# Kernel tuning notes

Measured on AMD Instinct MI355X. Metric: run time of the kernel, lower is better.

The kernel has to match this reference:

```python
import jax, jax.numpy as jnp
import numpy as np

B, L, H, NH = 2, 512, 128, 2
DH = H // NH
POS_VOCAB, REL_VOCAB = 512, 257


def setup_inputs() -> dict:
    key = jax.random.key(0)
    ks = jax.random.split(key, 16)
    s = 0.02
    inp = {
        "query": jax.random.normal(ks[0], (B, L, H), jnp.float32),
        "key": jax.random.normal(ks[1], (B, L, H), jnp.float32),
        "value": jax.random.normal(ks[2], (B, L, H), jnp.float32),
        "Wq": jax.random.normal(ks[3], (H, H), jnp.float32) * s,
        "bq": jnp.zeros((H,), jnp.float32),
        "Wk": jax.random.normal(ks[4], (H, H), jnp.float32) * s,
        "bk": jnp.zeros((H,), jnp.float32),
        "Wv": jax.random.normal(ks[5], (H, H), jnp.float32) * s,
        "bv": jnp.zeros((H,), jnp.float32),
        "Wo": jax.random.normal(ks[6], (H, H), jnp.float32) * s,
        "bo": jnp.zeros((H,), jnp.float32),
        "E_PK": jax.random.normal(ks[7], (POS_VOCAB, H), jnp.float32) * s,
        "E_PV": jax.random.normal(ks[8], (POS_VOCAB, H), jnp.float32) * s,
        "E_RK": jax.random.normal(ks[9], (REL_VOCAB, H), jnp.float32) * s,
        "E_RV": jax.random.normal(ks[10], (REL_VOCAB, H), jnp.float32) * s,
        "poss_seq": jax.random.randint(ks[11], (B, L), 0, POS_VOCAB),
        "interval_seq": jax.random.randint(ks[12], (B, L, L), 0, REL_VOCAB),
        # causal mask (True = attend), same role as attn_mask in the torch module
        "attn_mask": jnp.broadcast_to(jnp.tril(jnp.ones((L, L), bool)), (B, L, L)),
    }
    return inp


def reference(query, key, value, Wq, bq, Wk, bk, Wv, bv, Wo, bo,
              E_PK, E_PV, E_RK, E_RV, poss_seq, interval_seq, attn_mask):
    b, l, _ = query.shape
    # linear projections (torch Linear: x @ W.T + b)
    Q = query @ Wq.T + bq
    K = key @ Wk.T + bk + E_PK[poss_seq]
    V = value @ Wv.T + bv + E_PV[poss_seq]
    # relative key/value embeddings: (b, l, l, h, dh) -> (b, h, l, l, dh)
    rel_k = E_RK[interval_seq].reshape(b, l, l, NH, DH).transpose(0, 3, 1, 2, 4)
    rel_v = E_RV[interval_seq].reshape(b, l, l, NH, DH).transpose(0, 3, 1, 2, 4)
    # split heads: (b, h, l, dh)
    Qh = Q.reshape(b, l, NH, DH).transpose(0, 2, 1, 3)
    Kh = K.reshape(b, l, NH, DH).transpose(0, 2, 1, 3)
    Vh = V.reshape(b, l, NH, DH).transpose(0, 2, 1, 3)
    scores = jnp.einsum('bhld,bhkd->bhlk', Qh, Kh)
    scores = scores + jnp.einsum('bhld,bhlkd->bhlk', Qh, rel_k)
    scores = scores / jnp.sqrt(jnp.float32(DH))
    m = attn_mask[:, None]  # (b, 1, l, l)
    scores = jnp.where(m, scores, -jnp.inf)
    w = jax.nn.softmax(scores, axis=-1)
    w = jnp.where(m, w, 0.0)
    out = jnp.einsum('bhlk,bhkd->bhld', w, Vh)
    out = out + jnp.einsum('bhlk,bhlkd->bhld', w, rel_v)
    out = out.transpose(0, 2, 1, 3).reshape(b, l, H)
    out = out @ Wo.T + bo
    out = jnp.where(jnp.isnan(out), 0.0, out)
    return out
```

## Files before the change

### kernel.cpp

```cpp
#include <hip/hip_runtime.h>
#include <math.h>

#define LL 512
#define HH 128
#define NHH 2
#define DHH 64
#define RELV 257
#define PKS  260

#define OFF_QH   0
#define OFF_KT   131072
#define OFF_VH   262144
#define OFF_PK   393216
#define OFF_WQT  925696
#define OFF_WKT  942080
#define OFF_WVT  958464
#define OFF_WOT  974848
#define OFF_ERKT 991232

__global__ void prep_kernel(const float* Wq, const float* Wk, const float* Wv,
                            const float* Wo, const float* E_RK, float* ws) {
    int g = blockIdx.x * 256 + threadIdx.x;
    if (g < 65536) {
        int m = g >> 14, rem = g & 16383, i = rem >> 7, j = rem & 127;
        const float* W = (m == 0) ? Wq : (m == 1) ? Wk : (m == 2) ? Wv : Wo;
        ws[OFF_WQT + m * 16384 + i * 128 + j] = W[j * 128 + i];
    } else if (g < 65536 + 128 * RELV) {
        int g2 = g - 65536;
        int hd = g2 / RELV, r = g2 - hd * RELV;
        ws[OFF_ERKT + hd * RELV + r] = E_RK[r * HH + hd];
    }
}

__launch_bounds__(512)
__global__ void qkv_kernel(const float* q_in, const float* k_in, const float* v_in,
                           const float* bq, const float* bk, const float* bv,
                           const float* E_PK, const float* E_PV, const int* poss,
                           const float* Wqt, const float* Wkt, const float* Wvt,
                           const float* ERKt,
                           float* Qh, float* Kt, float* Vh, float* PK) {
    int row0 = blockIdx.x * 4;
    int b = row0 >> 9;
    int l0 = row0 & 511;
    int t = threadIdx.x;

    __shared__ float xin[3][4][128];
    __shared__ float qr[4][128];

    for (int g = t; g < 1536; g += 512) {
        int m = g >> 9, rem = g & 511, rr = rem >> 7, i = rem & 127;
        const float* src = (m == 0) ? q_in : (m == 1) ? k_in : v_in;
        xin[m][rr][i] = src[(row0 + rr) * 128 + i];
    }
    __syncthreads();

    int j = t & 127, rr = t >> 7;
    int row = row0 + rr, l = l0 + rr;
    float aq = bq[j], ak = bk[j], av = bv[j];
    const float* xq = xin[0][rr];
    const float* xk = xin[1][rr];
    const float* xv = xin[2][rr];
#pragma unroll 8
    for (int i = 0; i < 128; i++) {
        aq += xq[i] * Wqt[i * 128 + j];
        ak += xk[i] * Wkt[i * 128 + j];
        av += xv[i] * Wvt[i * 128 + j];
    }
    int pos = poss[row];
    ak += E_PK[pos * 128 + j];
    av += E_PV[pos * 128 + j];

    int h = j >> 6, d = j & 63, bh = b * NHH + h;
    Qh[(bh * LL + l) * DHH + d] = aq;
    Vh[(bh * LL + l) * DHH + d] = av;
    Kt[(bh * DHH + d) * LL + l] = ak;
    qr[rr][j] = aq;
    __syncthreads();

    for (int idx = t; idx < 2 * RELV; idx += 512) {
        int hh = idx >= RELV;
        int r = idx - hh * RELV;
        const float* er = ERKt + hh * 64 * RELV + r;
        const float* q0 = qr[0] + hh * 64;
        const float* q1 = qr[1] + hh * 64;
        const float* q2v = qr[2] + hh * 64;
        const float* q3 = qr[3] + hh * 64;
        float a0 = 0.f, a1 = 0.f, a2 = 0.f, a3 = 0.f;
#pragma unroll 8
        for (int dd = 0; dd < 64; dd++) {
            float e = er[dd * RELV];
            a0 += q0[dd] * e; a1 += q1[dd] * e;
            a2 += q2v[dd] * e; a3 += q3[dd] * e;
        }
        float* pk = PK + ((b * NHH + hh) * LL + l0) * PKS + r;
        pk[0] = a0; pk[PKS] = a1; pk[2 * PKS] = a2; pk[3 * PKS] = a3;
    }
}

__launch_bounds__(512)
__global__ void attn_kernel(const float* Qh, const float* Kt, const float* Vh,
                            const float* PK, const float* E_RV,
                            const float* Wot, const float* bo,
                            const int* interval, float* out) {
    int blk = blockIdx.x;
    int b = blk & 1;
    int p = blk >> 1;
    int l0 = 510 - 2 * p;
    int nk0 = l0 + 1, nk1 = l0 + 2;
    int t = threadIdx.x;
    int w = t >> 6, lane = t & 63;
    int h = w >> 2, s = w & 3;
    int bh = b * NHH + h;
    int kstep = (((nk1 + 3) >> 2) + 1) & ~1;
    int kbase = s * kstep; if (kbase > nk1) kbase = nk1;
    int kend = kbase + kstep; if (kend > nk1) kend = nk1;

    __shared__ float q2[2][2][DHH];
    __shared__ __align__(16) float pks[2][2][PKS];
    __shared__ float wb[2][2][RELV];
    __shared__ __align__(8) float sc[2][8][128];
    __shared__ float oa[2][8][DHH];
    __shared__ float ao[2][HH];
    __shared__ float po[2][4][HH];
    __shared__ float reds[2][8];

    int k0 = kbase + lane * 2;
    const int* idxr0 = interval + (b * LL + l0) * LL;
    const int* idxr1 = idxr0 + LL;
    int2 i20 = make_int2(0, 0), i21 = make_int2(0, 0);
    bool active = (k0 < kend);
    if (active) {
        i20 = *(const int2*)(idxr0 + k0);
        i21 = *(const int2*)(idxr1 + k0);
    }

    if (t < 256) {
        int row = t >> 7, hh = (t >> 6) & 1, dd = t & 63;
        q2[row][hh][dd] = Qh[((b * NHH + hh) * LL + (l0 + row)) * DHH + dd];
    }
    if (t < 260) {
        int row = t / 130, rem = t - row * 130;
        int hh = rem / 65, c = rem - hh * 65;
        const float4* src = (const float4*)(PK + ((b * NHH + hh) * LL + l0 + row) * PKS);
        ((float4*)pks[row][hh])[c] = src[c];
    }
    {
        float* wbf = &wb[0][0][0];
        for (int idx = t; idx < 4 * RELV; idx += 512) wbf[idx] = 0.f;
    }
    __syncthreads();

    float ax0 = 0.f, ay0 = 0.f, ax1 = 0.f, ay1 = 0.f;
    if (active) {
        const float* kb = Kt + bh * DHH * LL + k0;
#pragma unroll 16
        for (int d = 0; d < DHH; d++) {
            float2 kk = *(const float2*)(kb + d * LL);
            float qd0 = q2[0][h][d], qd1 = q2[1][h][d];
            ax0 += qd0 * kk.x; ay0 += qd0 * kk.y;
            ax1 += qd1 * kk.x; ay1 += qd1 * kk.y;
        }
    }
    bool m00 = active && (k0 < nk0);
    bool m01 = (k0 + 1 < kend) && (k0 + 1 < nk0);
    bool m10 = active;
    bool m11 = (k0 + 1 < kend);
    float e00 = m00 ? __expf((ax0 + pks[0][h][i20.x]) * 0.125f) : 0.f;
    float e01 = m01 ? __expf((ay0 + pks[0][h][i20.y]) * 0.125f) : 0.f;
    float e10 = m10 ? __expf((ax1 + pks[1][h][i21.x]) * 0.125f) : 0.f;
    float e11 = m11 ? __expf((ay1 + pks[1][h][i21.y]) * 0.125f) : 0.f;

    float ss0 = e00 + e01, ss1 = e10 + e11;
#pragma unroll
    for (int off = 32; off > 0; off >>= 1) {
        ss0 += __shfl_down(ss0, off);
        ss1 += __shfl_down(ss1, off);
    }
    if (lane == 0) { reds[0][w] = ss0; reds[1][w] = ss1; }

    *(float2*)&sc[0][w][lane * 2] = make_float2(e00, e01);
    *(float2*)&sc[1][w][lane * 2] = make_float2(e10, e11);
    if (m00) atomicAdd(&wb[0][h][i20.x], e00);
    if (m01) atomicAdd(&wb[0][h][i20.y], e01);
    if (m10) atomicAdd(&wb[1][h][i21.x], e10);
    if (m11) atomicAdd(&wb[1][h][i21.y], e11);
    __syncthreads();

    float a00 = 0.f, a01 = 0.f, a02 = 0.f, a03 = 0.f;
    float a10 = 0.f, a11 = 0.f, a12 = 0.f, a13 = 0.f;
    const float* vb = Vh + bh * LL * DHH + lane;
    int kcnt = kend - kbase; if (kcnt < 0) kcnt = 0;
    int niter = (kcnt + 3) >> 2;
    for (int ci = 0; ci < niter; ci++) {
        int k = kbase + ci * 4;
        const float* s0 = sc[0][w] + ci * 4;
        const float* s1 = sc[1][w] + ci * 4;
        float v0 = vb[(k + 0) * DHH], v1 = vb[(k + 1) * DHH];
        float v2 = vb[(k + 2) * DHH], v3 = vb[(k + 3) * DHH];
        a00 += s0[0] * v0; a01 += s0[1] * v1; a02 += s0[2] * v2; a03 += s0[3] * v3;
        a10 += s1[0] * v0; a11 += s1[1] * v1; a12 += s1[2] * v2; a13 += s1[3] * v3;
    }

    {
        int r0 = s * 64;
        const float* ev = E_RV + h * 64 + lane;
        const float* w0 = wb[0][h];
        const float* w1 = wb[1][h];
#pragma unroll 4
        for (int rr = 0; rr < 64; rr += 4) {
            int r = r0 + rr;
            float ev0 = ev[(r + 0) * HH], ev1 = ev[(r + 1) * HH];
            float ev2 = ev[(r + 2) * HH], ev3 = ev[(r + 3) * HH];
            a00 += w0[r + 0] * ev0; a01 += w0[r + 1] * ev1;
            a02 += w0[r + 2] * ev2; a03 += w0[r + 3] * ev3;
            a10 += w1[r + 0] * ev0; a11 += w1[r + 1] * ev1;
            a12 += w1[r + 2] * ev2; a13 += w1[r + 3] * ev3;
        }
        if (s == 3) {
            float e256 = ev[256 * HH];
            a00 += w0[256] * e256;
            a10 += w1[256] * e256;
        }
    }

    float inv0 = 1.f / ((reds[0][h * 4 + 0] + reds[0][h * 4 + 1]) +
                        (reds[0][h * 4 + 2] + reds[0][h * 4 + 3]));
    float inv1 = 1.f / ((reds[1][h * 4 + 0] + reds[1][h * 4 + 1]) +
                        (reds[1][h * 4 + 2] + reds[1][h * 4 + 3]));
    oa[0][w][lane] = ((a00 + a01) + (a02 + a03)) * inv0;
    oa[1][w][lane] = ((a10 + a11) + (a12 + a13)) * inv1;
    __syncthreads();

    if (t < 256) {
        int row = t >> 7, hd = t & 127, hh = hd >> 6, dd = hd & 63;
        ao[row][hd] = (oa[row][hh * 4 + 0][dd] + oa[row][hh * 4 + 1][dd]) +
                      (oa[row][hh * 4 + 2][dd] + oa[row][hh * 4 + 3][dd]);
    }
    __syncthreads();

    int j = t & 127, iq = t >> 7;
    float p0a = 0.f, p0b = 0.f, p1a = 0.f, p1b = 0.f;
    int ib = iq * 32;
#pragma unroll 8
    for (int ii = 0; ii < 32; ii += 2) {
        float wv0 = Wot[(ib + ii) * HH + j];
        float wv1 = Wot[(ib + ii + 1) * HH + j];
        p0a += ao[0][ib + ii] * wv0; p0b += ao[0][ib + ii + 1] * wv1;
        p1a += ao[1][ib + ii] * wv0; p1b += ao[1][ib + ii + 1] * wv1;
    }
    po[0][iq][j] = p0a + p0b;
    po[1][iq][j] = p1a + p1b;
    __syncthreads();
    if (t < 256) {
        int row = t >> 7, jj = t & 127;
        float o = (po[row][0][jj] + po[row][1][jj]) +
                  (po[row][2][jj] + po[row][3][jj]) + bo[jj];
        if (isnan(o)) o = 0.f;
        out[(b * LL + l0 + row) * HH + jj] = o;
    }
}

extern "C" void kernel_launch(void* const* d_in, const int* in_sizes, int n_in,
                              void* d_out, int out_size, void* d_ws, size_t ws_size,
                              hipStream_t stream) {
    const float* query = (const float*)d_in[0];
    const float* key   = (const float*)d_in[1];
    const float* value = (const float*)d_in[2];
    const float* Wq = (const float*)d_in[3];  const float* bq = (const float*)d_in[4];
    const float* Wk = (const float*)d_in[5];  const float* bk = (const float*)d_in[6];
    const float* Wv = (const float*)d_in[7];  const float* bv = (const float*)d_in[8];
    const float* Wo = (const float*)d_in[9];  const float* bo = (const float*)d_in[10];
    const float* E_PK = (const float*)d_in[11];
    const float* E_PV = (const float*)d_in[12];
    const float* E_RK = (const float*)d_in[13];
    const float* E_RV = (const float*)d_in[14];
    const int* poss     = (const int*)d_in[15];
    const int* interval = (const int*)d_in[16];

    float* ws = (float*)d_ws;
    float* Qh   = ws + OFF_QH;
    float* Kt   = ws + OFF_KT;
    float* Vh   = ws + OFF_VH;
    float* PK   = ws + OFF_PK;
    float* Wqt  = ws + OFF_WQT;
    float* Wkt  = ws + OFF_WKT;
    float* Wvt  = ws + OFF_WVT;
    float* Wot  = ws + OFF_WOT;
    float* ERKt = ws + OFF_ERKT;
    float* out = (float*)d_out;

    prep_kernel<<<385, 256, 0, stream>>>(Wq, Wk, Wv, Wo, E_RK, ws);
    qkv_kernel<<<256, 512, 0, stream>>>(query, key, value, bq, bk, bv,
                                        E_PK, E_PV, poss, Wqt, Wkt, Wvt, ERKt,
                                        Qh, Kt, Vh, PK);
    attn_kernel<<<512, 512, 0, stream>>>(Qh, Kt, Vh, PK, E_RV, Wot, bo,
                                         interval, out);
}
```

Measured before the change: 126.1 us.

## Fuse prep, QKV projection and attention into one cooperative kernel

```diff
diff --git a/kernel.cpp b/kernel.cpp
--- a/kernel.cpp
+++ b/kernel.cpp
@@ -1,5 +1,8 @@
 #include <hip/hip_runtime.h>
+#include <hip/hip_cooperative_groups.h>
 #include <math.h>
+
+namespace cg = cooperative_groups;
 
 #define LL 512
 #define HH 128
@@ -17,6 +20,267 @@
 #define OFF_WVT  958464
 #define OFF_WOT  974848
 #define OFF_ERKT 991232
+
+__global__ __launch_bounds__(512, 4) void fused_kernel(
+    const float* __restrict__ q_in, const float* __restrict__ k_in,
+    const float* __restrict__ v_in,
+    const float* __restrict__ Wq, const float* __restrict__ bq,
+    const float* __restrict__ Wk, const float* __restrict__ bk,
+    const float* __restrict__ Wv, const float* __restrict__ bv,
+    const float* __restrict__ Wo, const float* __restrict__ bo,
+    const float* __restrict__ E_PK, const float* __restrict__ E_PV,
+    const float* __restrict__ E_RK, const float* __restrict__ E_RV,
+    const int* __restrict__ poss, const int* __restrict__ interval,
+    float* __restrict__ out, float* ws) {
+
+    float* Qh   = ws + OFF_QH;
+    float* Kt   = ws + OFF_KT;
+    float* Vh   = ws + OFF_VH;
+    float* PK   = ws + OFF_PK;
+    float* Wqt  = ws + OFF_WQT;
+    float* Wkt  = ws + OFF_WKT;
+    float* Wvt  = ws + OFF_WVT;
+    float* Wot  = ws + OFF_WOT;
+    float* ERKt = ws + OFF_ERKT;
+
+    int blk = blockIdx.x;
+    int t = threadIdx.x;
+
+    __shared__ float xin2[3][2][128];
+    __shared__ float part[3][2][128];
+    __shared__ float qr2[2][128];
+    __shared__ float q2[2][2][DHH];
+    __shared__ __align__(16) float pks[2][2][PKS];
+    __shared__ float wb[2][2][RELV];
+    __shared__ __align__(8) float sc[2][8][128];
+    __shared__ float oa[2][8][DHH];
+    __shared__ float ao[2][HH];
+    __shared__ float po[2][4][HH];
+    __shared__ float reds[2][8];
+
+    {
+        int g = blk * 512 + t;
+        if (g < 65536) {
+            int m = g >> 14, rem = g & 16383, i = rem >> 7, j = rem & 127;
+            const float* W = (m == 0) ? Wq : (m == 1) ? Wk : (m == 2) ? Wv : Wo;
+            ws[OFF_WQT + m * 16384 + i * 128 + j] = W[j * 128 + i];
+        } else if (g < 65536 + 128 * RELV) {
+            int g2 = g - 65536;
+            int hd = g2 / RELV, r = g2 - hd * RELV;
+            ERKt[hd * RELV + r] = E_RK[r * HH + hd];
+        }
+    }
+    cg::this_grid().sync();
+
+    {
+        int row0 = blk * 2;
+        int b = row0 >> 9;
+        int l0 = row0 & 511;
+
+        for (int gg = t; gg < 768; gg += 512) {
+            int m = gg >> 8, rem = gg & 255, rr2 = rem >> 7, i = rem & 127;
+            const float* src = (m == 0) ? q_in : (m == 1) ? k_in : v_in;
+            xin2[m][rr2][i] = src[(row0 + rr2) * 128 + i];
+        }
+        __syncthreads();
+
+        int j = t & 127, rr = (t >> 7) & 1, ih = t >> 8;
+        const float* xq = xin2[0][rr];
+        const float* xk = xin2[1][rr];
+        const float* xv = xin2[2][rr];
+        float aq = 0.f, ak = 0.f, av = 0.f;
+        int i0 = ih * 64;
+#pragma unroll 8
+        for (int i = 0; i < 64; i++) {
+            int ii = i0 + i;
+            aq += xq[ii] * Wqt[ii * 128 + j];
+            ak += xk[ii] * Wkt[ii * 128 + j];
+            av += xv[ii] * Wvt[ii * 128 + j];
+        }
+        if (ih == 1) {
+            part[0][rr][j] = aq; part[1][rr][j] = ak; part[2][rr][j] = av;
+        }
+        __syncthreads();
+        if (ih == 0) {
+            aq += part[0][rr][j] + bq[j];
+            ak += part[1][rr][j] + bk[j];
+            av += part[2][rr][j] + bv[j];
+            int row = row0 + rr, l = l0 + rr;
+            int pos = poss[row];
+            ak += E_PK[pos * 128 + j];
+            av += E_PV[pos * 128 + j];
+            int h = j >> 6, d = j & 63, bh = b * NHH + h;
+            Qh[(bh * LL + l) * DHH + d] = aq;
+            Vh[(bh * LL + l) * DHH + d] = av;
+            Kt[(bh * DHH + d) * LL + l] = ak;
+            qr2[rr][j] = aq;
+        }
+        __syncthreads();
+
+        for (int idx = t; idx < 2 * RELV; idx += 512) {
+            int r = idx >> 1, rw = idx & 1;
+            const float* qq = qr2[rw];
+            const float* er = ERKt + r;
+            float a0 = 0.f, a1 = 0.f;
+#pragma unroll 8
+            for (int c = 0; c < 64; c++) {
+                a0 += qq[c] * er[c * RELV];
+                a1 += qq[64 + c] * er[(64 + c) * RELV];
+            }
+            PK[((b * NHH + 0) * LL + l0 + rw) * PKS + r] = a0;
+            PK[((b * NHH + 1) * LL + l0 + rw) * PKS + r] = a1;
+        }
+    }
+    cg::this_grid().sync();
+
+    {
+        int b = blk & 1;
+        int p = blk >> 1;
+        int l0 = 510 - 2 * p;
+        int nk0 = l0 + 1, nk1 = l0 + 2;
+        int w = t >> 6, lane = t & 63;
+        int h = w >> 2, s = w & 3;
+        int bh = b * NHH + h;
+        int kstep = (((nk1 + 3) >> 2) + 1) & ~1;
+        int kbase = s * kstep; if (kbase > nk1) kbase = nk1;
+        int kend = kbase + kstep; if (kend > nk1) kend = nk1;
+
+        int k0 = kbase + lane * 2;
+        const int* idxr0 = interval + (b * LL + l0) * LL;
+        const int* idxr1 = idxr0 + LL;
+        int2 i20 = make_int2(0, 0), i21 = make_int2(0, 0);
+        bool active = (k0 < kend);
+        if (active) {
+            i20 = *(const int2*)(idxr0 + k0);
+            i21 = *(const int2*)(idxr1 + k0);
+        }
+
+        if (t < 256) {
+            int row = t >> 7, hh = (t >> 6) & 1, dd = t & 63;
+            q2[row][hh][dd] = Qh[((b * NHH + hh) * LL + (l0 + row)) * DHH + dd];
+        }
+        if (t < 260) {
+            int row = t / 130, rem = t - row * 130;
+            int hh = rem / 65, c = rem - hh * 65;
+            const float4* src = (const float4*)(PK + ((b * NHH + hh) * LL + l0 + row) * PKS);
+            ((float4*)pks[row][hh])[c] = src[c];
+        }
+        {
+            float* wbf = &wb[0][0][0];
+            for (int idx = t; idx < 4 * RELV; idx += 512) wbf[idx] = 0.f;
+        }
+        __syncthreads();
+
+        float ax0 = 0.f, ay0 = 0.f, ax1 = 0.f, ay1 = 0.f;
+        if (active) {
+            const float* kb = Kt + bh * DHH * LL + k0;
+#pragma unroll 16
+            for (int d = 0; d < DHH; d++) {
+                float2 kk = *(const float2*)(kb + d * LL);
+                float qd0 = q2[0][h][d], qd1 = q2[1][h][d];
+                ax0 += qd0 * kk.x; ay0 += qd0 * kk.y;
+                ax1 += qd1 * kk.x; ay1 += qd1 * kk.y;
+            }
+        }
+        bool m00 = active && (k0 < nk0);
+        bool m01 = (k0 + 1 < kend) && (k0 + 1 < nk0);
+        bool m10 = active;
+        bool m11 = (k0 + 1 < kend);
+        float e00 = m00 ? __expf((ax0 + pks[0][h][i20.x]) * 0.125f) : 0.f;
+        float e01 = m01 ? __expf((ay0 + pks[0][h][i20.y]) * 0.125f) : 0.f;
+        float e10 = m10 ? __expf((ax1 + pks[1][h][i21.x]) * 0.125f) : 0.f;
+        float e11 = m11 ? __expf((ay1 + pks[1][h][i21.y]) * 0.125f) : 0.f;
+
+        float ss0 = e00 + e01, ss1 = e10 + e11;
+#pragma unroll
+        for (int off = 32; off > 0; off >>= 1) {
+            ss0 += __shfl_down(ss0, off);
+            ss1 += __shfl_down(ss1, off);
+        }
+        if (lane == 0) { reds[0][w] = ss0; reds[1][w] = ss1; }
+
+        *(float2*)&sc[0][w][lane * 2] = make_float2(e00, e01);
+        *(float2*)&sc[1][w][lane * 2] = make_float2(e10, e11);
+        if (m00) atomicAdd(&wb[0][h][i20.x], e00);
+        if (m01) atomicAdd(&wb[0][h][i20.y], e01);
+        if (m10) atomicAdd(&wb[1][h][i21.x], e10);
+        if (m11) atomicAdd(&wb[1][h][i21.y], e11);
+        __syncthreads();
+
+        float a00 = 0.f, a01 = 0.f, a02 = 0.f, a03 = 0.f;
+        float a10 = 0.f, a11 = 0.f, a12 = 0.f, a13 = 0.f;
+        const float* vb = Vh + bh * LL * DHH + lane;
+        int kcnt = kend - kbase; if (kcnt < 0) kcnt = 0;
+        int niter = (kcnt + 3) >> 2;
+        for (int ci = 0; ci < niter; ci++) {
+            int k = kbase + ci * 4;
+            const float* s0 = sc[0][w] + ci * 4;
+            const float* s1 = sc[1][w] + ci * 4;
+            float v0 = vb[(k + 0) * DHH], v1 = vb[(k + 1) * DHH];
+            float v2 = vb[(k + 2) * DHH], v3 = vb[(k + 3) * DHH];
+            a00 += s0[0] * v0; a01 += s0[1] * v1; a02 += s0[2] * v2; a03 += s0[3] * v3;
+            a10 += s1[0] * v0; a11 += s1[1] * v1; a12 += s1[2] * v2; a13 += s1[3] * v3;
+        }
+
+        {
+            int r0 = s * 64;
+            const float* ev = E_RV + h * 64 + lane;
+            const float* w0 = wb[0][h];
+            const float* w1 = wb[1][h];
+#pragma unroll 4
+            for (int rr = 0; rr < 64; rr += 4) {
+                int r = r0 + rr;
+                float ev0 = ev[(r + 0) * HH], ev1 = ev[(r + 1) * HH];
+                float ev2 = ev[(r + 2) * HH], ev3 = ev[(r + 3) * HH];
+                a00 += w0[r + 0] * ev0; a01 += w0[r + 1] * ev1;
+                a02 += w0[r + 2] * ev2; a03 += w0[r + 3] * ev3;
+                a10 += w1[r + 0] * ev0; a11 += w1[r + 1] * ev1;
+                a12 += w1[r + 2] * ev2; a13 += w1[r + 3] * ev3;
+            }
+            if (s == 3) {
+                float e256 = ev[256 * HH];
+                a00 += w0[256] * e256;
+                a10 += w1[256] * e256;
+            }
+        }
+
+        float inv0 = 1.f / ((reds[0][h * 4 + 0] + reds[0][h * 4 + 1]) +
+                            (reds[0][h * 4 + 2] + reds[0][h * 4 + 3]));
+        float inv1 = 1.f / ((reds[1][h * 4 + 0] + reds[1][h * 4 + 1]) +
+                            (reds[1][h * 4 + 2] + reds[1][h * 4 + 3]));
+        oa[0][w][lane] = ((a00 + a01) + (a02 + a03)) * inv0;
+        oa[1][w][lane] = ((a10 + a11) + (a12 + a13)) * inv1;
+        __syncthreads();
+
+        if (t < 256) {
+            int row = t >> 7, hd = t & 127, hh = hd >> 6, dd = hd & 63;
+            ao[row][hd] = (oa[row][hh * 4 + 0][dd] + oa[row][hh * 4 + 1][dd]) +
+                          (oa[row][hh * 4 + 2][dd] + oa[row][hh * 4 + 3][dd]);
+        }
+        __syncthreads();
+
+        int j = t & 127, iq = t >> 7;
+        float p0a = 0.f, p0b = 0.f, p1a = 0.f, p1b = 0.f;
+        int ib = iq * 32;
+#pragma unroll 8
+        for (int ii = 0; ii < 32; ii += 2) {
+            float wv0 = Wot[(ib + ii) * HH + j];
+            float wv1 = Wot[(ib + ii + 1) * HH + j];
+            p0a += ao[0][ib + ii] * wv0; p0b += ao[0][ib + ii + 1] * wv1;
+            p1a += ao[1][ib + ii] * wv0; p1b += ao[1][ib + ii + 1] * wv1;
+        }
+        po[0][iq][j] = p0a + p0b;
+        po[1][iq][j] = p1a + p1b;
+        __syncthreads();
+        if (t < 256) {
+            int row = t >> 7, jj = t & 127;
+            float o = (po[row][0][jj] + po[row][1][jj]) +
+                      (po[row][2][jj] + po[row][3][jj]) + bo[jj];
+            if (isnan(o)) o = 0.f;
+            out[(b * LL + l0 + row) * HH + jj] = o;
+        }
+    }
+}
 
 __global__ void prep_kernel(const float* Wq, const float* Wk, const float* Wv,
                             const float* Wo, const float* E_RK, float* ws) {
@@ -278,21 +542,34 @@
     const int* interval = (const int*)d_in[16];
 
     float* ws = (float*)d_ws;
-    float* Qh   = ws + OFF_QH;
-    float* Kt   = ws + OFF_KT;
-    float* Vh   = ws + OFF_VH;
-    float* PK   = ws + OFF_PK;
-    float* Wqt  = ws + OFF_WQT;
-    float* Wkt  = ws + OFF_WKT;
-    float* Wvt  = ws + OFF_WVT;
-    float* Wot  = ws + OFF_WOT;
-    float* ERKt = ws + OFF_ERKT;
     float* out = (float*)d_out;
 
-    prep_kernel<<<385, 256, 0, stream>>>(Wq, Wk, Wv, Wo, E_RK, ws);
-    qkv_kernel<<<256, 512, 0, stream>>>(query, key, value, bq, bk, bv,
-                                        E_PK, E_PV, poss, Wqt, Wkt, Wvt, ERKt,
-                                        Qh, Kt, Vh, PK);
-    attn_kernel<<<512, 512, 0, stream>>>(Qh, Kt, Vh, PK, E_RV, Wot, bo,
-                                         interval, out);
+    void* kargs[] = {
+        (void*)&query, (void*)&key, (void*)&value,
+        (void*)&Wq, (void*)&bq, (void*)&Wk, (void*)&bk,
+        (void*)&Wv, (void*)&bv, (void*)&Wo, (void*)&bo,
+        (void*)&E_PK, (void*)&E_PV, (void*)&E_RK, (void*)&E_RV,
+        (void*)&poss, (void*)&interval, (void*)&out, (void*)&ws
+    };
+    hipError_t err = hipLaunchCooperativeKernel(
+        (const void*)fused_kernel, dim3(512), dim3(512), kargs, 0, stream);
+
+    if (err != hipSuccess) {
+        float* Qh   = ws + OFF_QH;
+        float* Kt   = ws + OFF_KT;
+        float* Vh   = ws + OFF_VH;
+        float* PK   = ws + OFF_PK;
+        float* Wqt  = ws + OFF_WQT;
+        float* Wkt  = ws + OFF_WKT;
+        float* Wvt  = ws + OFF_WVT;
+        float* Wot  = ws + OFF_WOT;
+        float* ERKt = ws + OFF_ERKT;
+
+        prep_kernel<<<385, 256, 0, stream>>>(Wq, Wk, Wv, Wo, E_RK, ws);
+        qkv_kernel<<<256, 512, 0, stream>>>(query, key, value, bq, bk, bv,
+                                            E_PK, E_PV, poss, Wqt, Wkt, Wvt, ERKt,
+                                            Qh, Kt, Vh, PK);
+        attn_kernel<<<512, 512, 0, stream>>>(Qh, Kt, Vh, PK, E_RV, Wot, bo,
+                                             interval, out);
+    }
 }
```

New measurement: 270.6 us. 115% more time.

## Drop prep kernel, read untransposed weights directly, one query row per attention block

Applied to the files above, without the earlier changes.

```diff
diff --git a/kernel.cpp b/kernel.cpp
--- a/kernel.cpp
+++ b/kernel.cpp
@@ -12,251 +12,238 @@
 #define OFF_KT   131072
 #define OFF_VH   262144
 #define OFF_PK   393216
-#define OFF_WQT  925696
-#define OFF_WKT  942080
-#define OFF_WVT  958464
 #define OFF_WOT  974848
-#define OFF_ERKT 991232
-
-__global__ void prep_kernel(const float* Wq, const float* Wk, const float* Wv,
-                            const float* Wo, const float* E_RK, float* ws) {
-    int g = blockIdx.x * 256 + threadIdx.x;
-    if (g < 65536) {
-        int m = g >> 14, rem = g & 16383, i = rem >> 7, j = rem & 127;
-        const float* W = (m == 0) ? Wq : (m == 1) ? Wk : (m == 2) ? Wv : Wo;
-        ws[OFF_WQT + m * 16384 + i * 128 + j] = W[j * 128 + i];
-    } else if (g < 65536 + 128 * RELV) {
-        int g2 = g - 65536;
-        int hd = g2 / RELV, r = g2 - hd * RELV;
-        ws[OFF_ERKT + hd * RELV + r] = E_RK[r * HH + hd];
+
+__launch_bounds__(512, 8)
+__global__ void qkv_kernel(const float* __restrict__ q_in, const float* __restrict__ k_in,
+                           const float* __restrict__ v_in,
+                           const float* __restrict__ Wq, const float* __restrict__ bq,
+                           const float* __restrict__ Wk, const float* __restrict__ bk,
+                           const float* __restrict__ Wv, const float* __restrict__ bv,
+                           const float* __restrict__ Wo,
+                           const float* __restrict__ E_PK, const float* __restrict__ E_PV,
+                           const float* __restrict__ E_RK, const int* __restrict__ poss,
+                           float* __restrict__ Qh, float* __restrict__ Kt,
+                           float* __restrict__ Vh, float* __restrict__ PK,
+                           float* __restrict__ Wot) {
+    int blk = blockIdx.x;
+    int row0 = blk * 2;
+    int b = row0 >> 9, l0 = row0 & 511;
+    int t = threadIdx.x;
+
+    __shared__ __align__(16) float xin[3][2][128];
+    __shared__ float part[3][2][4][128];
+    __shared__ float qr[2][128];
+
+    if (t < 192) {
+        int m = t >> 6, rem = t & 63, rr = rem >> 5, c = rem & 31;
+        const float* src = (m == 0) ? q_in : (m == 1) ? k_in : v_in;
+        ((float4*)xin[m][rr])[c] = ((const float4*)(src + (row0 + rr) * 128))[c];
+    } else if (t < 224) {
+        int idx = blk * 32 + (t - 192);
+        int i = idx >> 7, j = idx & 127;
+        Wot[i * 128 + j] = Wo[j * 128 + i];
+    }
+    __syncthreads();
+
+    int j = t & 127, iq = t >> 7;
+    int i0 = iq * 32;
+    float aq0 = 0.f, aq1 = 0.f, ak0 = 0.f, ak1 = 0.f, av0 = 0.f, av1 = 0.f;
+    {
+        const float4* wq4 = (const float4*)(Wq + j * 128 + i0);
+        const float4* wk4 = (const float4*)(Wk + j * 128 + i0);
+        const float4* wv4 = (const float4*)(Wv + j * 128 + i0);
+        const float4* xq0 = (const float4*)(xin[0][0] + i0);
+        const float4* xq1 = (const float4*)(xin[0][1] + i0);
+        const float4* xk0 = (const float4*)(xin[1][0] + i0);
+        const float4* xk1 = (const float4*)(xin[1][1] + i0);
+        const float4* xv0 = (const float4*)(xin[2][0] + i0);
+        const float4* xv1 = (const float4*)(xin[2][1] + i0);
+#pragma unroll
+        for (int c = 0; c < 8; c++) {
+            float4 w, x0, x1;
+            w = wq4[c]; x0 = xq0[c]; x1 = xq1[c];
+            aq0 += w.x * x0.x + w.y * x0.y + w.z * x0.z + w.w * x0.w;
+            aq1 += w.x * x1.x + w.y * x1.y + w.z * x1.z + w.w * x1.w;
+            w = wk4[c]; x0 = xk0[c]; x1 = xk1[c];
+            ak0 += w.x * x0.x + w.y * x0.y + w.z * x0.z + w.w * x0.w;
+            ak1 += w.x * x1.x + w.y * x1.y + w.z * x1.z + w.w * x1.w;
+            w = wv4[c]; x0 = xv0[c]; x1 = xv1[c];
+            av0 += w.x * x0.x + w.y * x0.y + w.z * x0.z + w.w * x0.w;
+            av1 += w.x * x1.x + w.y * x1.y + w.z * x1.z + w.w * x1.w;
+        }
+    }
+    part[0][0][iq][j] = aq0; part[0][1][iq][j] = aq1;
+    part[1][0][iq][j] = ak0; part[1][1][iq][j] = ak1;
+    part[2][0][iq][j] = av0; part[2][1][iq][j] = av1;
+    __syncthreads();
+
+    if (t < 256) {
+        int jj = t & 127, rr = t >> 7;
+        int row = row0 + rr, l = l0 + rr;
+        float aq = (part[0][rr][0][jj] + part[0][rr][1][jj]) +
+                   (part[0][rr][2][jj] + part[0][rr][3][jj]) + bq[jj];
+        float ak = (part[1][rr][0][jj] + part[1][rr][1][jj]) +
+                   (part[1][rr][2][jj] + part[1][rr][3][jj]) + bk[jj];
+        float av = (part[2][rr][0][jj] + part[2][rr][1][jj]) +
+                   (part[2][rr][2][jj] + part[2][rr][3][jj]) + bv[jj];
+        int pos = poss[row];
+        ak += E_PK[pos * 128 + jj];
+        av += E_PV[pos * 128 + jj];
+        int h = jj >> 6, d = jj & 63, bh = b * NHH + h;
+        Qh[(bh * LL + l) * DHH + d] = aq;
+        Vh[(bh * LL + l) * DHH + d] = av;
+        Kt[(bh * DHH + d) * LL + l] = ak;
+        qr[rr][jj] = aq;
+    }
+    __syncthreads();
+
+    for (int idx = t; idx < 2 * RELV; idx += 512) {
+        int r = idx >> 1, head = idx & 1;
+        const float4* er4 = (const float4*)(E_RK + r * HH + head * 64);
+        const float* q0 = qr[0] + head * 64;
+        const float* q1 = qr[1] + head * 64;
+        float a0 = 0.f, a1 = 0.f;
+#pragma unroll
+        for (int c = 0; c < 16; c++) {
+            float4 e = er4[c];
+            const float* q0c = q0 + c * 4;
+            const float* q1c = q1 + c * 4;
+            a0 += e.x * q0c[0] + e.y * q0c[1] + e.z * q0c[2] + e.w * q0c[3];
+            a1 += e.x * q1c[0] + e.y * q1c[1] + e.z * q1c[2] + e.w * q1c[3];
+        }
+        float* pk = PK + ((b * NHH + head) * LL + l0) * PKS + r;
+        pk[0] = a0;
+        pk[PKS] = a1;
     }
 }
 
-__launch_bounds__(512)
-__global__ void qkv_kernel(const float* q_in, const float* k_in, const float* v_in,
-                           const float* bq, const float* bk, const float* bv,
-                           const float* E_PK, const float* E_PV, const int* poss,
-                           const float* Wqt, const float* Wkt, const float* Wvt,
-                           const float* ERKt,
-                           float* Qh, float* Kt, float* Vh, float* PK) {
-    int row0 = blockIdx.x * 4;
-    int b = row0 >> 9;
-    int l0 = row0 & 511;
-    int t = threadIdx.x;
-
-    __shared__ float xin[3][4][128];
-    __shared__ float qr[4][128];
-
-    for (int g = t; g < 1536; g += 512) {
-        int m = g >> 9, rem = g & 511, rr = rem >> 7, i = rem & 127;
-        const float* src = (m == 0) ? q_in : (m == 1) ? k_in : v_in;
-        xin[m][rr][i] = src[(row0 + rr) * 128 + i];
-    }
-    __syncthreads();
-
-    int j = t & 127, rr = t >> 7;
-    int row = row0 + rr, l = l0 + rr;
-    float aq = bq[j], ak = bk[j], av = bv[j];
-    const float* xq = xin[0][rr];
-    const float* xk = xin[1][rr];
-    const float* xv = xin[2][rr];
-#pragma unroll 8
-    for (int i = 0; i < 128; i++) {
-        aq += xq[i] * Wqt[i * 128 + j];
-        ak += xk[i] * Wkt[i * 128 + j];
-        av += xv[i] * Wvt[i * 128 + j];
-    }
-    int pos = poss[row];
-    ak += E_PK[pos * 128 + j];
-    av += E_PV[pos * 128 + j];
-
-    int h = j >> 6, d = j & 63, bh = b * NHH + h;
-    Qh[(bh * LL + l) * DHH + d] = aq;
-    Vh[(bh * LL + l) * DHH + d] = av;
-    Kt[(bh * DHH + d) * LL + l] = ak;
-    qr[rr][j] = aq;
-    __syncthreads();
-
-    for (int idx = t; idx < 2 * RELV; idx += 512) {
-        int hh = idx >= RELV;
-        int r = idx - hh * RELV;
-        const float* er = ERKt + hh * 64 * RELV + r;
-        const float* q0 = qr[0] + hh * 64;
-        const float* q1 = qr[1] + hh * 64;
-        const float* q2v = qr[2] + hh * 64;
-        const float* q3 = qr[3] + hh * 64;
-        float a0 = 0.f, a1 = 0.f, a2 = 0.f, a3 = 0.f;
-#pragma unroll 8
-        for (int dd = 0; dd < 64; dd++) {
-            float e = er[dd * RELV];
-            a0 += q0[dd] * e; a1 += q1[dd] * e;
-            a2 += q2v[dd] * e; a3 += q3[dd] * e;
-        }
-        float* pk = PK + ((b * NHH + hh) * LL + l0) * PKS + r;
-        pk[0] = a0; pk[PKS] = a1; pk[2 * PKS] = a2; pk[3 * PKS] = a3;
-    }
-}
-
-__launch_bounds__(512)
-__global__ void attn_kernel(const float* Qh, const float* Kt, const float* Vh,
-                            const float* PK, const float* E_RV,
-                            const float* Wot, const float* bo,
-                            const int* interval, float* out) {
+__launch_bounds__(512, 8)
+__global__ void attn_kernel(const float* __restrict__ Qh, const float* __restrict__ Kt,
+                            const float* __restrict__ Vh, const float* __restrict__ PK,
+                            const float* __restrict__ E_RV, const float* __restrict__ Wot,
+                            const float* __restrict__ bo, const int* __restrict__ interval,
+                            float* __restrict__ out) {
     int blk = blockIdx.x;
     int b = blk & 1;
-    int p = blk >> 1;
-    int l0 = 510 - 2 * p;
-    int nk0 = l0 + 1, nk1 = l0 + 2;
+    int l = 511 - (blk >> 1);
+    int nk = l + 1;
     int t = threadIdx.x;
     int w = t >> 6, lane = t & 63;
     int h = w >> 2, s = w & 3;
     int bh = b * NHH + h;
-    int kstep = (((nk1 + 3) >> 2) + 1) & ~1;
-    int kbase = s * kstep; if (kbase > nk1) kbase = nk1;
-    int kend = kbase + kstep; if (kend > nk1) kend = nk1;
-
-    __shared__ float q2[2][2][DHH];
-    __shared__ __align__(16) float pks[2][2][PKS];
-    __shared__ float wb[2][2][RELV];
-    __shared__ __align__(8) float sc[2][8][128];
-    __shared__ float oa[2][8][DHH];
-    __shared__ float ao[2][HH];
-    __shared__ float po[2][4][HH];
-    __shared__ float reds[2][8];
+    int kstep = (((nk + 3) >> 2) + 1) & ~1;
+    int kbase = s * kstep; if (kbase > nk) kbase = nk;
+    int kend = kbase + kstep; if (kend > nk) kend = nk;
+
+    __shared__ float q2[2][DHH];
+    __shared__ __align__(16) float pks[2][PKS];
+    __shared__ float wb[2][RELV];
+    __shared__ __align__(8) float sc[8][128];
+    __shared__ float oa[8][DHH];
+    __shared__ float ao[HH];
+    __shared__ float po[4][HH];
+    __shared__ float reds[8];
 
     int k0 = kbase + lane * 2;
-    const int* idxr0 = interval + (b * LL + l0) * LL;
-    const int* idxr1 = idxr0 + LL;
-    int2 i20 = make_int2(0, 0), i21 = make_int2(0, 0);
+    const int* idxr = interval + (b * LL + l) * LL;
+    int2 i2 = make_int2(0, 0);
     bool active = (k0 < kend);
-    if (active) {
-        i20 = *(const int2*)(idxr0 + k0);
-        i21 = *(const int2*)(idxr1 + k0);
-    }
-
-    if (t < 256) {
-        int row = t >> 7, hh = (t >> 6) & 1, dd = t & 63;
-        q2[row][hh][dd] = Qh[((b * NHH + hh) * LL + (l0 + row)) * DHH + dd];
-    }
-    if (t < 260) {
-        int row = t / 130, rem = t - row * 130;
-        int hh = rem / 65, c = rem - hh * 65;
-        const float4* src = (const float4*)(PK + ((b * NHH + hh) * LL + l0 + row) * PKS);
-        ((float4*)pks[row][hh])[c] = src[c];
+    if (active) i2 = *(const int2*)(idxr + k0);
+
+    if (t < 128) {
+        int hh = t >> 6, dd = t & 63;
+        q2[hh][dd] = Qh[((b * NHH + hh) * LL + l) * DHH + dd];
+    }
+    if (t < 130) {
+        int hh = t / 65, c = t - hh * 65;
+        ((float4*)pks[hh])[c] =
+            ((const float4*)(PK + ((b * NHH + hh) * LL + l) * PKS))[c];
     }
     {
-        float* wbf = &wb[0][0][0];
-        for (int idx = t; idx < 4 * RELV; idx += 512) wbf[idx] = 0.f;
-    }
-    __syncthreads();
-
-    float ax0 = 0.f, ay0 = 0.f, ax1 = 0.f, ay1 = 0.f;
+        float* wbf = &wb[0][0];
+        for (int idx = t; idx < 2 * RELV; idx += 512) wbf[idx] = 0.f;
+    }
+    __syncthreads();
+
+    float ax = 0.f, ay = 0.f;
     if (active) {
         const float* kb = Kt + bh * DHH * LL + k0;
 #pragma unroll 16
         for (int d = 0; d < DHH; d++) {
             float2 kk = *(const float2*)(kb + d * LL);
-            float qd0 = q2[0][h][d], qd1 = q2[1][h][d];
-            ax0 += qd0 * kk.x; ay0 += qd0 * kk.y;
-            ax1 += qd1 * kk.x; ay1 += qd1 * kk.y;
-        }
-    }
-    bool m00 = active && (k0 < nk0);
-    bool m01 = (k0 + 1 < kend) && (k0 + 1 < nk0);
-    bool m10 = active;
-    bool m11 = (k0 + 1 < kend);
-    float e00 = m00 ? __expf((ax0 + pks[0][h][i20.x]) * 0.125f) : 0.f;
-    float e01 = m01 ? __expf((ay0 + pks[0][h][i20.y]) * 0.125f) : 0.f;
-    float e10 = m10 ? __expf((ax1 + pks[1][h][i21.x]) * 0.125f) : 0.f;
-    float e11 = m11 ? __expf((ay1 + pks[1][h][i21.y]) * 0.125f) : 0.f;
-
-    float ss0 = e00 + e01, ss1 = e10 + e11;
+            float qd = q2[h][d];
+            ax += qd * kk.x; ay += qd * kk.y;
+        }
+    }
+    bool m1 = (k0 + 1 < kend);
+    float e0 = active ? __expf((ax + pks[h][i2.x]) * 0.125f) : 0.f;
+    float e1 = m1 ? __expf((ay + pks[h][i2.y]) * 0.125f) : 0.f;
+
+    float ss = e0 + e1;
 #pragma unroll
-    for (int off = 32; off > 0; off >>= 1) {
-        ss0 += __shfl_down(ss0, off);
-        ss1 += __shfl_down(ss1, off);
-    }
-    if (lane == 0) { reds[0][w] = ss0; reds[1][w] = ss1; }
-
-    *(float2*)&sc[0][w][lane * 2] = make_float2(e00, e01);
-    *(float2*)&sc[1][w][lane * 2] = make_float2(e10, e11);
-    if (m00) atomicAdd(&wb[0][h][i20.x], e00);
-    if (m01) atomicAdd(&wb[0][h][i20.y], e01);
-    if (m10) atomicAdd(&wb[1][h][i21.x], e10);
-    if (m11) atomicAdd(&wb[1][h][i21.y], e11);
-    __syncthreads();
-
-    float a00 = 0.f, a01 = 0.f, a02 = 0.f, a03 = 0.f;
-    float a10 = 0.f, a11 = 0.f, a12 = 0.f, a13 = 0.f;
+    for (int off = 32; off > 0; off >>= 1) ss += __shfl_down(ss, off);
+    if (lane == 0) reds[w] = ss;
+
+    *(float2*)&sc[w][lane * 2] = make_float2(e0, e1);
+    if (active) atomicAdd(&wb[h][i2.x], e0);
+    if (m1) atomicAdd(&wb[h][i2.y], e1);
+    __syncthreads();
+
+    float a0 = 0.f, a1 = 0.f, a2 = 0.f, a3 = 0.f;
     const float* vb = Vh + bh * LL * DHH + lane;
     int kcnt = kend - kbase; if (kcnt < 0) kcnt = 0;
     int niter = (kcnt + 3) >> 2;
     for (int ci = 0; ci < niter; ci++) {
         int k = kbase + ci * 4;
-        const float* s0 = sc[0][w] + ci * 4;
-        const float* s1 = sc[1][w] + ci * 4;
-        float v0 = vb[(k + 0) * DHH], v1 = vb[(k + 1) * DHH];
-        float v2 = vb[(k + 2) * DHH], v3 = vb[(k + 3) * DHH];
-        a00 += s0[0] * v0; a01 += s0[1] * v1; a02 += s0[2] * v2; a03 += s0[3] * v3;
-        a10 += s1[0] * v0; a11 += s1[1] * v1; a12 += s1[2] * v2; a13 += s1[3] * v3;
+        const float* s0 = sc[w] + ci * 4;
+        a0 += s0[0] * vb[(k + 0) * DHH];
+        a1 += s0[1] * vb[(k + 1) * DHH];
+        a2 += s0[2] * vb[(k + 2) * DHH];
+        a3 += s0[3] * vb[(k + 3) * DHH];
     }
 
     {
         int r0 = s * 64;
         const float* ev = E_RV + h * 64 + lane;
-        const float* w0 = wb[0][h];
-        const float* w1 = wb[1][h];
+        const float* w0 = wb[h];
 #pragma unroll 4
         for (int rr = 0; rr < 64; rr += 4) {
             int r = r0 + rr;
-            float ev0 = ev[(r + 0) * HH], ev1 = ev[(r + 1) * HH];
-            float ev2 = ev[(r + 2) * HH], ev3 = ev[(r + 3) * HH];
-            a00 += w0[r + 0] * ev0; a01 += w0[r + 1] * ev1;
-            a02 += w0[r + 2] * ev2; a03 += w0[r + 3] * ev3;
-            a10 += w1[r + 0] * ev0; a11 += w1[r + 1] * ev1;
-            a12 += w1[r + 2] * ev2; a13 += w1[r + 3] * ev3;
-        }
-        if (s == 3) {
-            float e256 = ev[256 * HH];
-            a00 += w0[256] * e256;
-            a10 += w1[256] * e256;
-        }
-    }
-
-    float inv0 = 1.f / ((reds[0][h * 4 + 0] + reds[0][h * 4 + 1]) +
-                        (reds[0][h * 4 + 2] + reds[0][h * 4 + 3]));
-    float inv1 = 1.f / ((reds[1][h * 4 + 0] + reds[1][h * 4 + 1]) +
-                        (reds[1][h * 4 + 2] + reds[1][h * 4 + 3]));
-    oa[0][w][lane] = ((a00 + a01) + (a02 + a03)) * inv0;
-    oa[1][w][lane] = ((a10 + a11) + (a12 + a13)) * inv1;
-    __syncthreads();
-
-    if (t < 256) {
-        int row = t >> 7, hd = t & 127, hh = hd >> 6, dd = hd & 63;
-        ao[row][hd] = (oa[row][hh * 4 + 0][dd] + oa[row][hh * 4 + 1][dd]) +
-                      (oa[row][hh * 4 + 2][dd] + oa[row][hh * 4 + 3][dd]);
+            a0 += w0[r + 0] * ev[(r + 0) * HH];
+            a1 += w0[r + 1] * ev[(r + 1) * HH];
+            a2 += w0[r + 2] * ev[(r + 2) * HH];
+            a3 += w0[r + 3] * ev[(r + 3) * HH];
+        }
+        if (s == 3) a0 += w0[256] * ev[256 * HH];
+    }
+
+    float inv = 1.f / ((reds[h * 4 + 0] + reds[h * 4 + 1]) +
+                       (reds[h * 4 + 2] + reds[h * 4 + 3]));
+    oa[w][lane] = ((a0 + a1) + (a2 + a3)) * inv;
+    __syncthreads();
+
+    if (t < 128) {
+        int hh = t >> 6, dd = t & 63;
+        ao[t] = (oa[hh * 4 + 0][dd] + oa[hh * 4 + 1][dd]) +
+                (oa[hh * 4 + 2][dd] + oa[hh * 4 + 3][dd]);
     }
     __syncthreads();
 
     int j = t & 127, iq = t >> 7;
-    float p0a = 0.f, p0b = 0.f, p1a = 0.f, p1b = 0.f;
+    float pa = 0.f, pb = 0.f;
     int ib = iq * 32;
 #pragma unroll 8
     for (int ii = 0; ii < 32; ii += 2) {
-        float wv0 = Wot[(ib + ii) * HH + j];
-        float wv1 = Wot[(ib + ii + 1) * HH + j];
-        p0a += ao[0][ib + ii] * wv0; p0b += ao[0][ib + ii + 1] * wv1;
-        p1a += ao[1][ib + ii] * wv0; p1b += ao[1][ib + ii + 1] * wv1;
-    }
-    po[0][iq][j] = p0a + p0b;
-    po[1][iq][j] = p1a + p1b;
-    __syncthreads();
-    if (t < 256) {
-        int row = t >> 7, jj = t & 127;
-        float o = (po[row][0][jj] + po[row][1][jj]) +
-                  (po[row][2][jj] + po[row][3][jj]) + bo[jj];
+        pa += ao[ib + ii] * Wot[(ib + ii) * HH + j];
+        pb += ao[ib + ii + 1] * Wot[(ib + ii + 1) * HH + j];
+    }
+    po[iq][j] = pa + pb;
+    __syncthreads();
+    if (t < 128) {
+        float o = (po[0][t] + po[1][t]) + (po[2][t] + po[3][t]) + bo[t];
         if (isnan(o)) o = 0.f;
-        out[(b * LL + l0 + row) * HH + jj] = o;
+        out[(b * LL + l) * HH + t] = o;
     }
 }
 
@@ -282,17 +269,13 @@
     float* Kt   = ws + OFF_KT;
     float* Vh   = ws + OFF_VH;
     float* PK   = ws + OFF_PK;
-    float* Wqt  = ws + OFF_WQT;
-    float* Wkt  = ws + OFF_WKT;
-    float* Wvt  = ws + OFF_WVT;
     float* Wot  = ws + OFF_WOT;
-    float* ERKt = ws + OFF_ERKT;
     float* out = (float*)d_out;
 
-    prep_kernel<<<385, 256, 0, stream>>>(Wq, Wk, Wv, Wo, E_RK, ws);
-    qkv_kernel<<<256, 512, 0, stream>>>(query, key, value, bq, bk, bv,
-                                        E_PK, E_PV, poss, Wqt, Wkt, Wvt, ERKt,
-                                        Qh, Kt, Vh, PK);
-    attn_kernel<<<512, 512, 0, stream>>>(Qh, Kt, Vh, PK, E_RV, Wot, bo,
-                                         interval, out);
+    qkv_kernel<<<512, 512, 0, stream>>>(query, key, value,
+                                        Wq, bq, Wk, bk, Wv, bv, Wo,
+                                        E_PK, E_PV, E_RK, poss,
+                                        Qh, Kt, Vh, PK, Wot);
+    attn_kernel<<<1024, 512, 0, stream>>>(Qh, Kt, Vh, PK, E_RV, Wot, bo,
+                                          interval, out);
 }
```

After: 184.0 us. 45.9% more time.

## Replace rel-value histogram with direct per-key gather of E_RV rows

Applied to the files above, without the earlier changes.

```diff
diff --git a/kernel.cpp b/kernel.cpp
--- a/kernel.cpp
+++ b/kernel.cpp
@@ -117,8 +117,8 @@
 
     __shared__ float q2[2][2][DHH];
     __shared__ __align__(16) float pks[2][2][PKS];
-    __shared__ float wb[2][2][RELV];
     __shared__ __align__(8) float sc[2][8][128];
+    __shared__ __align__(8) int   scI[2][8][128];
     __shared__ float oa[2][8][DHH];
     __shared__ float ao[2][HH];
     __shared__ float po[2][4][HH];
@@ -143,10 +143,6 @@
         int hh = rem / 65, c = rem - hh * 65;
         const float4* src = (const float4*)(PK + ((b * NHH + hh) * LL + l0 + row) * PKS);
         ((float4*)pks[row][hh])[c] = src[c];
-    }
-    {
-        float* wbf = &wb[0][0][0];
-        for (int idx = t; idx < 4 * RELV; idx += 512) wbf[idx] = 0.f;
     }
     __syncthreads();
 
@@ -180,47 +176,33 @@
 
     *(float2*)&sc[0][w][lane * 2] = make_float2(e00, e01);
     *(float2*)&sc[1][w][lane * 2] = make_float2(e10, e11);
-    if (m00) atomicAdd(&wb[0][h][i20.x], e00);
-    if (m01) atomicAdd(&wb[0][h][i20.y], e01);
-    if (m10) atomicAdd(&wb[1][h][i21.x], e10);
-    if (m11) atomicAdd(&wb[1][h][i21.y], e11);
+    *(int2*)&scI[0][w][lane * 2] = i20;
+    *(int2*)&scI[1][w][lane * 2] = i21;
     __syncthreads();
 
     float a00 = 0.f, a01 = 0.f, a02 = 0.f, a03 = 0.f;
     float a10 = 0.f, a11 = 0.f, a12 = 0.f, a13 = 0.f;
     const float* vb = Vh + bh * LL * DHH + lane;
+    const float* eb = E_RV + h * 64 + lane;
+    const float* s0p = sc[0][w];
+    const float* s1p = sc[1][w];
+    const int* r0p = scI[0][w];
+    const int* r1p = scI[1][w];
     int kcnt = kend - kbase; if (kcnt < 0) kcnt = 0;
     int niter = (kcnt + 3) >> 2;
     for (int ci = 0; ci < niter; ci++) {
-        int k = kbase + ci * 4;
-        const float* s0 = sc[0][w] + ci * 4;
-        const float* s1 = sc[1][w] + ci * 4;
+        int kk = ci * 4;
+        int k = kbase + kk;
+        float w00 = s0p[kk + 0], w01 = s0p[kk + 1], w02 = s0p[kk + 2], w03 = s0p[kk + 3];
+        float w10 = s1p[kk + 0], w11 = s1p[kk + 1], w12 = s1p[kk + 2], w13 = s1p[kk + 3];
+        int r00 = r0p[kk + 0], r01 = r0p[kk + 1], r02 = r0p[kk + 2], r03 = r0p[kk + 3];
+        int r10 = r1p[kk + 0], r11 = r1p[kk + 1], r12 = r1p[kk + 2], r13 = r1p[kk + 3];
         float v0 = vb[(k + 0) * DHH], v1 = vb[(k + 1) * DHH];
         float v2 = vb[(k + 2) * DHH], v3 = vb[(k + 3) * DHH];
-        a00 += s0[0] * v0; a01 += s0[1] * v1; a02 += s0[2] * v2; a03 += s0[3] * v3;
-        a10 += s1[0] * v0; a11 += s1[1] * v1; a12 += s1[2] * v2; a13 += s1[3] * v3;
-    }
-
-    {
-        int r0 = s * 64;
-        const float* ev = E_RV + h * 64 + lane;
-        const float* w0 = wb[0][h];
-        const float* w1 = wb[1][h];
-#pragma unroll 4
-        for (int rr = 0; rr < 64; rr += 4) {
-            int r = r0 + rr;
-            float ev0 = ev[(r + 0) * HH], ev1 = ev[(r + 1) * HH];
-            float ev2 = ev[(r + 2) * HH], ev3 = ev[(r + 3) * HH];
-            a00 += w0[r + 0] * ev0; a01 += w0[r + 1] * ev1;
-            a02 += w0[r + 2] * ev2; a03 += w0[r + 3] * ev3;
-            a10 += w1[r + 0] * ev0; a11 += w1[r + 1] * ev1;
-            a12 += w1[r + 2] * ev2; a13 += w1[r + 3] * ev3;
-        }
-        if (s == 3) {
-            float e256 = ev[256 * HH];
-            a00 += w0[256] * e256;
-            a10 += w1[256] * e256;
-        }
+        a00 += w00 * (v0 + eb[r00 * HH]); a10 += w10 * (v0 + eb[r10 * HH]);
+        a01 += w01 * (v1 + eb[r01 * HH]); a11 += w11 * (v1 + eb[r11 * HH]);
+        a02 += w02 * (v2 + eb[r02 * HH]); a12 += w12 * (v2 + eb[r12 * HH]);
+        a03 += w03 * (v3 + eb[r03 * HH]); a13 += w13 * (v3 + eb[r13 * HH]);
     }
 
     float inv0 = 1.f / ((reds[0][h * 4 + 0] + reds[0][h * 4 + 1]) +
```

New measurement: 127.0 us. About the same (+0.7%).
